# Kernel tuning notes

Hardware: AMD Instinct MI355X
Metric: run time of the kernel (lower is better)

Reference implementation:

```python
import jax, jax.numpy as jnp
import numpy as np

N_QUBITS = 10
DIM = 2 ** N_QUBITS
N_TOKENS = 32
LAYERS = 2
DEGREE = 3
VOCAB = 32000
EMB = 512
N_PARAMS = 4 * N_QUBITS * LAYERS      # angles per token circuit
N_PARAMS_FF = 4 * N_QUBITS            # quantum feedforward (1 layer)
BATCH = 32


def _ry(state, wire, theta, n):
    # state: [B, 2**n] complex64; theta: [B] float32. RY = [[c,-s],[s,c]], c=cos(th/2)
    st = state.reshape(-1, 2 ** wire, 2, 2 ** (n - wire - 1))
    c = jnp.cos(theta / 2)[:, None, None]
    s = jnp.sin(theta / 2)[:, None, None]
    a, b = st[:, :, 0, :], st[:, :, 1, :]
    st = jnp.stack([c * a - s * b, s * a + c * b], axis=2)
    return st.reshape(-1, 2 ** n)


def _crx(state, ctrl, tgt, theta, n):
    # controlled-RX: apply RX=[[c,-i s],[-i s,c]] on tgt where ctrl bit == 1
    lo, hi = (ctrl, tgt) if ctrl < tgt else (tgt, ctrl)
    st = state.reshape(-1, 2 ** lo, 2, 2 ** (hi - lo - 1), 2, 2 ** (n - hi - 1))
    caxis = 2 if ctrl < tgt else 4
    taxis = 4 if ctrl < tgt else 2
    c = jnp.cos(theta / 2).reshape(-1, 1, 1, 1, 1, 1)
    s = jnp.sin(theta / 2).reshape(-1, 1, 1, 1, 1, 1)
    c0 = jax.lax.index_in_dim(st, 0, caxis, keepdims=True)
    c1 = jax.lax.index_in_dim(st, 1, caxis, keepdims=True)
    a = jax.lax.index_in_dim(c1, 0, taxis, keepdims=True)
    b = jax.lax.index_in_dim(c1, 1, taxis, keepdims=True)
    na = c * a - 1j * s * b
    nb = -1j * s * a + c * b
    c1 = jnp.concatenate([na, nb], axis=taxis)
    st = jnp.concatenate([c0, c1], axis=caxis)
    return st.reshape(-1, 2 ** n)


def _ansatz14(state, params, n, layers):
    # gate order of ansatz 14 (arXiv:1905.10876); params: [B, 4*n*layers]
    idx = 0
    for _ in range(layers):
        for i in range(n):
            state = _ry(state, i, params[:, idx], n); idx += 1
        for i in range(n - 1, -1, -1):
            state = _crx(state, i, (i + 1) % n, params[:, idx], n); idx += 1
        for i in range(n):
            state = _ry(state, i, params[:, idx], n); idx += 1
        for i in [n - 1] + list(range(n - 1)):
            state = _crx(state, i, (i - 1) % n, params[:, idx], n); idx += 1
    return state


def _measure_xyz(state, n):
    # expectation of X,Y,Z on every wire; output [B, 3*n] ordered [x..., y..., z...]
    B = state.shape[0]
    xs, ys, zs = [], [], []
    for w in range(n):
        st = state.reshape(B, 2 ** w, 2, 2 ** (n - w - 1))
        a, b = st[:, :, 0, :], st[:, :, 1, :]
        z = jnp.sum(jnp.conj(a) * b, axis=(1, 2))
        xs.append(2.0 * jnp.real(z))
        ys.append(2.0 * jnp.imag(z))
        zs.append(jnp.sum(jnp.real(a * jnp.conj(a)) - jnp.real(b * jnp.conj(b)), axis=(1, 2)))
    return jnp.stack(xs + ys + zs, axis=1)


def _forward(x, emb, w_ang, b_ang, qsvt_coeffs, lcu_re, lcu_im, qff_params, w1, b1, w2, b2):
    B, T = x.shape
    lcu = (lcu_re + 1j * lcu_im).astype(jnp.complex64)
    lcu = lcu / jnp.maximum(jnp.sum(jnp.abs(lcu)), 1e-12)          # p=1 normalize
    angles = (emb[x] @ w_ang.T + b_ang).reshape(B * T, N_PARAMS)   # [B*T, P]
    init = jnp.zeros((B, DIM), jnp.complex64).at[:, 0].set(1.0)
    acc = qsvt_coeffs[0] * init
    mono = init
    for k in range(1, DEGREE + 1):
        rep = jnp.repeat(mono, T, axis=0)                          # [B*T, D]
        st = _ansatz14(rep, angles, N_QUBITS, LAYERS).reshape(B, T, DIM)
        mono = jnp.einsum('bwi,w->bi', st, lcu)                    # LCU combine
        acc = acc + qsvt_coeffs[k] * mono
    qsvt_state = acc / jnp.sum(jnp.abs(qsvt_coeffs))
    norm = jnp.linalg.norm(qsvt_state, axis=-1, keepdims=True)
    normed = qsvt_state / jnp.maximum(norm, 1e-12)
    qff = jnp.broadcast_to(qff_params[None, :], (B, N_PARAMS_FF))
    st2 = _ansatz14(normed, qff, N_QUBITS, 1)
    ev = _measure_xyz(st2, N_QUBITS)                               # [B, 3*nq]
    h = jax.nn.relu(ev @ w1.T + b1)
    logits = h @ w2.T + b2
    return logits, jnp.mean(norm[:, 0])


def setup_inputs() -> dict:
    key = jax.random.key(0)
    ks = jax.random.split(key, 9)
    return {
        'x': jax.random.randint(ks[0], (BATCH, N_TOKENS), 0, VOCAB, dtype=jnp.int32),
        'emb': jax.random.normal(ks[1], (VOCAB, EMB), jnp.float32) * 0.02,
        'w_ang': jax.random.normal(ks[2], (N_PARAMS, EMB), jnp.float32) * (1.0 / np.sqrt(EMB)),
        'b_ang': jnp.zeros((N_PARAMS,), jnp.float32),
        'qsvt_coeffs': jax.random.uniform(ks[3], (DEGREE + 1,), jnp.float32),
        'lcu_re': jax.random.uniform(ks[4], (N_TOKENS,), jnp.float32),
        'lcu_im': jax.random.uniform(ks[5], (N_TOKENS,), jnp.float32),
        'qff_params': jax.random.uniform(ks[6], (N_PARAMS_FF,), jnp.float32),
        'w1': jax.random.normal(ks[7], (EMB, 3 * N_QUBITS), jnp.float32) * (1.0 / np.sqrt(3 * N_QUBITS)),
        'b1': jnp.zeros((EMB,), jnp.float32),
        'w2': jax.random.normal(ks[8], (VOCAB, EMB), jnp.float32) * (1.0 / np.sqrt(EMB)),
        'b2': jnp.zeros((VOCAB,), jnp.float32),
    }


def reference(x, emb, w_ang, b_ang, qsvt_coeffs, lcu_re, lcu_im, qff_params, w1, b1, w2, b2):
    return _forward(x, emb, w_ang, b_ang, qsvt_coeffs, lcu_re, lcu_im, qff_params, w1, b1, w2, b2)
```

## Files before the change

### kernel.cpp

```cpp
#include <hip/hip_runtime.h>
#include <math.h>

#define DEV __device__ __forceinline__

namespace {

struct C2 { float x, y; };

constexpr size_t OFF_CS   = 0;
constexpr size_t OFF_NRM  = 163988;
constexpr size_t OFF_MONO = 164096;
constexpr size_t OFF_ACC  = 229632;
constexpr size_t OFF_ST   = 295168;
constexpr size_t OFF_H    = 2393280;


template<int P>
DEV void ry_gate(C2 v[16], int lane, float c, float s) {
  if constexpr (P >= 6) {
    constexpr int rm = 1 << (P - 6);
#pragma unroll
    for (int r = 0; r < 16; ++r) {
      if ((r & rm) == 0) {
        C2 a = v[r], b = v[r | rm];
        v[r].x      = fmaf(c, a.x, -s * b.x);
        v[r].y      = fmaf(c, a.y, -s * b.y);
        v[r | rm].x = fmaf(s, a.x,  c * b.x);
        v[r | rm].y = fmaf(s, a.y,  c * b.y);
      }
    }
  } else {
    constexpr int lm = 1 << P;
    float sg = (lane & lm) ? s : -s;
#pragma unroll
    for (int r = 0; r < 16; ++r) {
      float px = __shfl_xor(v[r].x, lm, 64);
      float py = __shfl_xor(v[r].y, lm, 64);
      v[r].x = fmaf(c, v[r].x, sg * px);
      v[r].y = fmaf(c, v[r].y, sg * py);
    }
  }
}

template<int PC, int PT>
DEV void crx_gate(C2 v[16], int lane, float c, float s) {
  if constexpr (PT >= 6) {
    constexpr int tm = 1 << (PT - 6);
#pragma unroll
    for (int r = 0; r < 16; ++r) {
      if ((r & tm) == 0) {
        if constexpr (PC >= 6) {
          constexpr int cm = 1 << (PC - 6);
          if ((r & cm) != 0) {
            C2 a = v[r], b = v[r | tm];
            v[r].x      = fmaf(c, a.x,  s * b.y);
            v[r].y      = fmaf(c, a.y, -s * b.x);
            v[r | tm].x = fmaf(c, b.x,  s * a.y);
            v[r | tm].y = fmaf(c, b.y, -s * a.x);
          }
        } else {
          constexpr int cl = 1 << PC;
          bool ct = (lane & cl) != 0;
          C2 a = v[r], b = v[r | tm];
          float nax = fmaf(c, a.x,  s * b.y);
          float nay = fmaf(c, a.y, -s * b.x);
          float nbx = fmaf(c, b.x,  s * a.y);
          float nby = fmaf(c, b.y, -s * a.x);
          v[r].x      = ct ? nax : a.x;
          v[r].y      = ct ? nay : a.y;
          v[r | tm].x = ct ? nbx : b.x;
          v[r | tm].y = ct ? nby : b.y;
        }
      }
    }
  } else {
    constexpr int tm = 1 << PT;
#pragma unroll
    for (int r = 0; r < 16; ++r) {
      if constexpr (PC >= 6) {
        constexpr int cm = 1 << (PC - 6);
        if ((r & cm) == 0) continue;
      }
      float px = __shfl_xor(v[r].x, tm, 64);
      float py = __shfl_xor(v[r].y, tm, 64);
      float nx = fmaf(c, v[r].x,  s * py);
      float ny = fmaf(c, v[r].y, -s * px);
      if constexpr (PC >= 6) {
        v[r].x = nx; v[r].y = ny;
      } else {
        constexpr int cl = 1 << PC;
        bool ct = (lane & cl) != 0;
        v[r].x = ct ? nx : v[r].x;
        v[r].y = ct ? ny : v[r].y;
      }
    }
  }
}

#define RYG(w, g)       ry_gate<9-(w)>(v, lane, cs[2*(g)], cs[2*(g)+1])
#define CRXG(cw, tw, g) crx_gate<9-(cw), 9-(tw)>(v, lane, cs[2*(g)], cs[2*(g)+1])

DEV void apply_layer(C2 v[16], int lane, const float* __restrict__ cs) {
  RYG(0,0); RYG(1,1); RYG(2,2); RYG(3,3); RYG(4,4);
  RYG(5,5); RYG(6,6); RYG(7,7); RYG(8,8); RYG(9,9);
  CRXG(9,0,10); CRXG(8,9,11); CRXG(7,8,12); CRXG(6,7,13); CRXG(5,6,14);
  CRXG(4,5,15); CRXG(3,4,16); CRXG(2,3,17); CRXG(1,2,18); CRXG(0,1,19);
  RYG(0,20); RYG(1,21); RYG(2,22); RYG(3,23); RYG(4,24);
  RYG(5,25); RYG(6,26); RYG(7,27); RYG(8,28); RYG(9,29);
  CRXG(9,8,30); CRXG(0,9,31); CRXG(1,0,32); CRXG(2,1,33); CRXG(3,2,34);
  CRXG(4,3,35); CRXG(5,4,36); CRXG(6,5,37); CRXG(7,6,38); CRXG(8,7,39);
}

template<int P>
DEV void measure_wire(const C2 v[16], int lane, float* ev, int w) {
  float x = 0.f, y = 0.f, z = 0.f;
  if constexpr (P >= 6) {
    constexpr int rm = 1 << (P - 6);
#pragma unroll
    for (int r = 0; r < 16; ++r) {
      if ((r & rm) == 0) {
        C2 a = v[r], b = v[r | rm];
        x += a.x*b.x + a.y*b.y;
        y += a.x*b.y - a.y*b.x;
        z += (a.x*a.x + a.y*a.y) - (b.x*b.x + b.y*b.y);
      }
    }
  } else {
    constexpr int lm = 1 << P;
#pragma unroll
    for (int r = 0; r < 16; ++r) {
      float px = __shfl_xor(v[r].x, lm, 64);
      float py = __shfl_xor(v[r].y, lm, 64);
      if ((lane & lm) == 0) {
        C2 a = v[r];
        x += a.x*px + a.y*py;
        y += a.x*py - a.y*px;
        z += (a.x*a.x + a.y*a.y) - (px*px + py*py);
      }
    }
  }
  for (int s = 1; s < 64; s <<= 1) {
    x += __shfl_xor(x, s, 64);
    y += __shfl_xor(y, s, 64);
    z += __shfl_xor(z, s, 64);
  }
  if (lane == 0) {
    ev[w]      = 2.f * x;
    ev[10 + w] = 2.f * y;
    ev[20 + w] = z;
  }
}

DEV void measure_all(const C2 v[16], int lane, float* ev) {
  measure_wire<9>(v, lane, ev, 0);
  measure_wire<8>(v, lane, ev, 1);
  measure_wire<7>(v, lane, ev, 2);
  measure_wire<6>(v, lane, ev, 3);
  measure_wire<5>(v, lane, ev, 4);
  measure_wire<4>(v, lane, ev, 5);
  measure_wire<3>(v, lane, ev, 6);
  measure_wire<2>(v, lane, ev, 7);
  measure_wire<1>(v, lane, ev, 8);
  measure_wire<0>(v, lane, ev, 9);
}


__global__ __launch_bounds__(128) void k_angles(const int* __restrict__ x,
                                                const float* __restrict__ emb,
                                                const float* __restrict__ w_ang,
                                                const float* __restrict__ b_ang,
                                                float* __restrict__ ws) {
  __shared__ float4 e4[4][128];
  int g = blockIdx.x;
  int tid = threadIdx.x;
#pragma unroll
  for (int rr = 0; rr < 4; ++rr) {
    int row = x[4 * g + rr];
    e4[rr][tid] = ((const float4*)(emb + (size_t)row * 512))[tid];
  }
  __syncthreads();
  if (tid < 80) {
    const float4* wr = (const float4*)(w_ang + (size_t)tid * 512);
    float bv = b_ang[tid];
    float a0 = bv, a1 = bv, a2 = bv, a3 = bv;
#pragma unroll 4
    for (int j = 0; j < 128; ++j) {
      float4 w = wr[j];
      float4 e0 = e4[0][j], e1 = e4[1][j], e2 = e4[2][j], e3 = e4[3][j];
      a0 = fmaf(w.x, e0.x, a0); a0 = fmaf(w.y, e0.y, a0);
      a0 = fmaf(w.z, e0.z, a0); a0 = fmaf(w.w, e0.w, a0);
      a1 = fmaf(w.x, e1.x, a1); a1 = fmaf(w.y, e1.y, a1);
      a1 = fmaf(w.z, e1.z, a1); a1 = fmaf(w.w, e1.w, a1);
      a2 = fmaf(w.x, e2.x, a2); a2 = fmaf(w.y, e2.y, a2);
      a2 = fmaf(w.z, e2.z, a2); a2 = fmaf(w.w, e2.w, a2);
      a3 = fmaf(w.x, e3.x, a3); a3 = fmaf(w.y, e3.y, a3);
      a3 = fmaf(w.z, e3.z, a3); a3 = fmaf(w.w, e3.w, a3);
    }
    float t0 = 0.5f * a0, t1 = 0.5f * a1, t2 = 0.5f * a2, t3 = 0.5f * a3;
    size_t base = OFF_CS + (size_t)(4 * g) * 160 + 2 * tid;
    ws[base]           = cosf(t0); ws[base + 1]       = sinf(t0);
    ws[base + 160]     = cosf(t1); ws[base + 161]     = sinf(t1);
    ws[base + 320]     = cosf(t2); ws[base + 321]     = sinf(t2);
    ws[base + 480]     = cosf(t3); ws[base + 481]     = sinf(t3);
  }
}

__global__ __launch_bounds__(256) void k_evolve(float* __restrict__ ws,
                                                const float* __restrict__ lr,
                                                const float* __restrict__ li,
                                                int k) {
  __shared__ float cs_lds[640];
  int tid = threadIdx.x;
  const float* csg = ws + OFF_CS + (size_t)blockIdx.x * 640;
  for (int i = tid; i < 640; i += 256) cs_lds[i] = csg[i];
  __syncthreads();
  int wid = tid >> 6, lane = tid & 63;
  int state = blockIdx.x * 4 + wid;
  int b = state >> 5, t = state & 31;

  float lre_v = 0.f, lim_v = 0.f;
  if (lane < 32) { lre_v = lr[lane]; lim_v = li[lane]; }
  float ab = sqrtf(lre_v * lre_v + lim_v * lim_v);
  for (int s = 1; s < 64; s <<= 1) ab += __shfl_xor(ab, s, 64);
  float invL = 1.f / fmaxf(ab, 1e-12f);
  float wre = __shfl(lre_v, t, 64) * invL;
  float wim = __shfl(lim_v, t, 64) * invL;

  C2 v[16];
  if (k == 1) {
#pragma unroll
    for (int r = 0; r < 16; ++r) {
      v[r].x = (r == 0 && lane == 0) ? 1.f : 0.f;
      v[r].y = 0.f;
    }
  } else {
    const float2* mono = (const float2*)(ws + OFF_MONO) + (size_t)b * 1024;
#pragma unroll
    for (int r = 0; r < 16; ++r) {
      float2 m = mono[(r << 6) | lane];
      v[r].x = m.x; v[r].y = m.y;
    }
  }
  const float* csw = &cs_lds[wid * 160];
  apply_layer(v, lane, csw);
  apply_layer(v, lane, csw + 80);
  float2* st = (float2*)(ws + OFF_ST) + (size_t)state * 1024;
#pragma unroll
  for (int r = 0; r < 16; ++r) {
    st[(r << 6) | lane] = make_float2(wre * v[r].x - wim * v[r].y,
                                      wre * v[r].y + wim * v[r].x);
  }
}

__global__ void k_reduce(float* __restrict__ ws, const float* __restrict__ coef, int k) {
  int idx = blockIdx.x * 256 + threadIdx.x;
  int b = idx >> 10, i = idx & 1023;
  const float2* st = (const float2*)(ws + OFF_ST) + (size_t)b * 32768 + i;
  float sx = 0.f, sy = 0.f;
#pragma unroll
  for (int t = 0; t < 32; ++t) {
    float2 vv = st[t * 1024];
    sx += vv.x; sy += vv.y;
  }
  float2* mono = (float2*)(ws + OFF_MONO);
  float2* acc  = (float2*)(ws + OFF_ACC);
  float ck = coef[k];
  if (k == 1) {
    float e0 = (i == 0) ? coef[0] : 0.f;
    acc[idx] = make_float2(fmaf(ck, sx, e0), ck * sy);
    mono[idx] = make_float2(sx, sy);
  } else {
    float2 a = acc[idx];
    a.x = fmaf(ck, sx, a.x);
    a.y = fmaf(ck, sy, a.y);
    acc[idx] = a;
    mono[idx] = make_float2(sx, sy);
  }
}

__global__ __launch_bounds__(256) void k_final(float* __restrict__ ws,
                                               const float* __restrict__ coef,
                                               const float* __restrict__ qff,
                                               const float* __restrict__ w1,
                                               const float* __restrict__ b1) {
  __shared__ float qff_lds[80];
  __shared__ float2 sv[1024];
  __shared__ float ev_lds[30];
  int tid = threadIdx.x;
  int b = blockIdx.x;
  if (tid < 40) {
    float th = 0.5f * qff[tid];
    qff_lds[2 * tid]     = cosf(th);
    qff_lds[2 * tid + 1] = sinf(th);
  }
  float den = fabsf(coef[0]) + fabsf(coef[1]) + fabsf(coef[2]) + fabsf(coef[3]);
  float invd = 1.f / den;
  float c3 = coef[3];
  const float2* stb  = (const float2*)(ws + OFF_ST) + (size_t)b * 32768;
  const float2* accb = (const float2*)(ws + OFF_ACC) + (size_t)b * 1024;
#pragma unroll
  for (int q = 0; q < 4; ++q) {
    int i = tid + q * 256;
    float sx = 0.f, sy = 0.f;
#pragma unroll
    for (int t = 0; t < 32; ++t) {
      float2 vv = stb[t * 1024 + i];
      sx += vv.x; sy += vv.y;
    }
    float2 a = accb[i];
    sv[i] = make_float2(fmaf(c3, sx, a.x) * invd, fmaf(c3, sy, a.y) * invd);
  }
  __syncthreads();
  if (tid < 64) {
    int lane = tid;
    C2 v[16];
    float ssum = 0.f;
#pragma unroll
    for (int r = 0; r < 16; ++r) {
      float2 m = sv[(r << 6) | lane];
      v[r].x = m.x; v[r].y = m.y;
      ssum += v[r].x * v[r].x + v[r].y * v[r].y;
    }
    for (int s = 1; s < 64; s <<= 1) ssum += __shfl_xor(ssum, s, 64);
    float nrm = sqrtf(ssum);
    if (lane == 0) ws[OFF_NRM + b] = nrm;
    float sc = 1.f / fmaxf(nrm, 1e-12f);
#pragma unroll
    for (int r = 0; r < 16; ++r) { v[r].x *= sc; v[r].y *= sc; }
    apply_layer(v, lane, qff_lds);
    measure_all(v, lane, ev_lds);
  }
  __syncthreads();
#pragma unroll
  for (int jj = 0; jj < 2; ++jj) {
    int j = tid + jj * 256;
    const float* wr = w1 + (size_t)j * 30;
    float a = b1[j];
#pragma unroll
    for (int q = 0; q < 30; ++q) a = fmaf(ev_lds[q], wr[q], a);
    ws[OFF_H + b * 512 + j] = fmaxf(a, 0.f);
  }
}

__global__ __launch_bounds__(256) void k_logits(const float* __restrict__ ws,
                                                const float* __restrict__ w2,
                                                const float* __restrict__ b2,
                                                float* __restrict__ out) {
  __shared__ float4 hT[4096];
  int tid = threadIdx.x;
  if (blockIdx.x == 0 && tid == 0) {
    float s = 0.f;
    for (int i = 0; i < 32; ++i) s += ws[OFF_NRM + i];
    out[32000u * 32u] = s * (1.f / 32.f);
  }
  const float4* hg = (const float4*)(ws + OFF_H);
#pragma unroll
  for (int p = 0; p < 16; ++p) {
    int idx = tid + p * 256;
    int m = idx >> 7, kf4 = idx & 127;
    hT[m * 128 + (kf4 ^ (m >> 3))] = hg[idx];
  }
  __syncthreads();

  int wv = tid >> 6, lane = tid & 63;
  int mg = lane & 3, nl = lane >> 2;
  int nbase = blockIdx.x * 64;
  float acc[4][8];
#pragma unroll
  for (int j = 0; j < 4; ++j)
#pragma unroll
    for (int mi = 0; mi < 8; ++mi) acc[j][mi] = 0.f;

  const float* wbase = w2 + (size_t)(nbase + nl * 4) * 512 + wv * 128;
  int kqb = wv * 32;
#pragma unroll 2
  for (int kf4 = 0; kf4 < 32; ++kf4) {
    int kcol = kqb + kf4;
    float4 h4[8];
#pragma unroll
    for (int mi = 0; mi < 8; ++mi) {
      int m = mg * 8 + mi;
      h4[mi] = hT[m * 128 + (kcol ^ mg)];
    }
#pragma unroll
    for (int j = 0; j < 4; ++j) {
      float4 w4 = *(const float4*)(wbase + (size_t)j * 512 + kf4 * 4);
#pragma unroll
      for (int mi = 0; mi < 8; ++mi) {
        acc[j][mi] = fmaf(w4.x, h4[mi].x, acc[j][mi]);
        acc[j][mi] = fmaf(w4.y, h4[mi].y, acc[j][mi]);
        acc[j][mi] = fmaf(w4.z, h4[mi].z, acc[j][mi]);
        acc[j][mi] = fmaf(w4.w, h4[mi].w, acc[j][mi]);
      }
    }
  }

  __syncthreads();
#pragma unroll
  for (int mi = 0; mi < 8; ++mi) {
    hT[wv * 512 + lane * 8 + (mi ^ (lane & 7))] =
        make_float4(acc[0][mi], acc[1][mi], acc[2][mi], acc[3][mi]);
  }
  __syncthreads();
  {
    int lane2 = tid & 63, grp = tid >> 6;
    int mg2 = lane2 & 3, nl2 = lane2 >> 2;
#pragma unroll
    for (int jj = 0; jj < 2; ++jj) {
      int mi2 = grp * 2 + jj;
      float4 s0 = hT[0 * 512 + lane2 * 8 + (mi2 ^ (lane2 & 7))];
      float4 s1 = hT[1 * 512 + lane2 * 8 + (mi2 ^ (lane2 & 7))];
      float4 s2 = hT[2 * 512 + lane2 * 8 + (mi2 ^ (lane2 & 7))];
      float4 s3 = hT[3 * 512 + lane2 * 8 + (mi2 ^ (lane2 & 7))];
      float sx = s0.x + s1.x + s2.x + s3.x;
      float sy = s0.y + s1.y + s2.y + s3.y;
      float sz = s0.z + s1.z + s2.z + s3.z;
      float sw = s0.w + s1.w + s2.w + s3.w;
      int m = mg2 * 8 + mi2;
      int col = nbase + nl2 * 4;
      float4 b2v = *(const float4*)(b2 + col);
      float4 res = make_float4(sx + b2v.x, sy + b2v.y, sz + b2v.z, sw + b2v.w);
      *(float4*)(out + (size_t)m * 32000 + col) = res;
    }
  }
}

}

extern "C" void kernel_launch(void* const* d_in, const int* in_sizes, int n_in,
                              void* d_out, int out_size, void* d_ws, size_t ws_size,
                              hipStream_t stream) {
  (void)in_sizes; (void)n_in; (void)out_size; (void)ws_size;
  const int*   x    = (const int*)d_in[0];
  const float* emb  = (const float*)d_in[1];
  const float* wang = (const float*)d_in[2];
  const float* bang = (const float*)d_in[3];
  const float* coef = (const float*)d_in[4];
  const float* lre  = (const float*)d_in[5];
  const float* lim  = (const float*)d_in[6];
  const float* qff  = (const float*)d_in[7];
  const float* w1   = (const float*)d_in[8];
  const float* b1   = (const float*)d_in[9];
  const float* w2   = (const float*)d_in[10];
  const float* b2   = (const float*)d_in[11];
  float* out = (float*)d_out;
  float* ws  = (float*)d_ws;

  hipLaunchKernelGGL(k_angles, dim3(256), dim3(128), 0, stream, x, emb, wang, bang, ws);
  hipLaunchKernelGGL(k_evolve, dim3(256), dim3(256), 0, stream, ws, lre, lim, 1);
  hipLaunchKernelGGL(k_reduce, dim3(128), dim3(256), 0, stream, ws, coef, 1);
  hipLaunchKernelGGL(k_evolve, dim3(256), dim3(256), 0, stream, ws, lre, lim, 2);
  hipLaunchKernelGGL(k_reduce, dim3(128), dim3(256), 0, stream, ws, coef, 2);
  hipLaunchKernelGGL(k_evolve, dim3(256), dim3(256), 0, stream, ws, lre, lim, 3);
  hipLaunchKernelGGL(k_final,  dim3(32),  dim3(256), 0, stream, ws, coef, qff, w1, b1);
  hipLaunchKernelGGL(k_logits, dim3(500), dim3(256), 0, stream, ws, w2, b2, out);
}
```

Before: 165.4 us.

## Split each state across two wavefronts and fuse angle computation into first evolve

Each 1024-amplitude state now spans two wavefronts (8 registers per lane instead of 16), with top-wire gates handled by exchanging halves through shared memory behind block barriers. The angle projection kernel is folded into the first evolve launch, which computes cos/sin into LDS and also writes them to the workspace for later passes. This doubles the thread count per state and cuts register pressure, trading that for extra LDS traffic and __syncthreads per layer, and it removes one launch.

```diff
diff --git a/kernel.cpp b/kernel.cpp
--- a/kernel.cpp
+++ b/kernel.cpp
@@ -13,7 +13,6 @@
 constexpr size_t OFF_ACC  = 229632;
 constexpr size_t OFF_ST   = 295168;
 constexpr size_t OFF_H    = 2393280;
-
 
 template<int P>
 DEV void ry_gate(C2 v[16], int lane, float c, float s) {
@@ -165,58 +164,253 @@
 }
 
 
-__global__ __launch_bounds__(128) void k_angles(const int* __restrict__ x,
-                                                const float* __restrict__ emb,
-                                                const float* __restrict__ w_ang,
-                                                const float* __restrict__ b_ang,
-                                                float* __restrict__ ws) {
-  __shared__ float4 e4[4][128];
-  int g = blockIdx.x;
-  int tid = threadIdx.x;
-#pragma unroll
-  for (int rr = 0; rr < 4; ++rr) {
-    int row = x[4 * g + rr];
-    e4[rr][tid] = ((const float4*)(emb + (size_t)row * 512))[tid];
-  }
+template<int P>
+DEV void ry8(C2 v[8], int lane, float c, float s) {
+  if constexpr (P >= 6) {
+    constexpr int rm = 1 << (P - 6);
+#pragma unroll
+    for (int r = 0; r < 8; ++r) {
+      if ((r & rm) == 0) {
+        C2 a = v[r], b = v[r | rm];
+        v[r].x      = fmaf(c, a.x, -s * b.x);
+        v[r].y      = fmaf(c, a.y, -s * b.y);
+        v[r | rm].x = fmaf(s, a.x,  c * b.x);
+        v[r | rm].y = fmaf(s, a.y,  c * b.y);
+      }
+    }
+  } else {
+    constexpr int lm = 1 << P;
+    float sg = (lane & lm) ? s : -s;
+#pragma unroll
+    for (int r = 0; r < 8; ++r) {
+      float px = __shfl_xor(v[r].x, lm, 64);
+      float py = __shfl_xor(v[r].y, lm, 64);
+      v[r].x = fmaf(c, v[r].x, sg * px);
+      v[r].y = fmaf(c, v[r].y, sg * py);
+    }
+  }
+}
+
+template<int PT>
+DEV void rx_all8(C2 v[8], int lane, float c, float s) {
+  if constexpr (PT >= 6) {
+    constexpr int tm = 1 << (PT - 6);
+#pragma unroll
+    for (int r = 0; r < 8; ++r) {
+      if ((r & tm) == 0) {
+        C2 a = v[r], bb = v[r | tm];
+        v[r].x      = fmaf(c, a.x,  s * bb.y);
+        v[r].y      = fmaf(c, a.y, -s * bb.x);
+        v[r | tm].x = fmaf(c, bb.x,  s * a.y);
+        v[r | tm].y = fmaf(c, bb.y, -s * a.x);
+      }
+    }
+  } else {
+    constexpr int tm = 1 << PT;
+#pragma unroll
+    for (int r = 0; r < 8; ++r) {
+      float px = __shfl_xor(v[r].x, tm, 64);
+      float py = __shfl_xor(v[r].y, tm, 64);
+      v[r].x = fmaf(c, v[r].x,  s * py);
+      v[r].y = fmaf(c, v[r].y, -s * px);
+    }
+  }
+}
+
+template<int PC, int PT>
+DEV void crx8(C2 v[8], int lane, int half, float c, float s) {
+  if constexpr (PC == 9) {
+    if (half) rx_all8<PT>(v, lane, c, s);
+  } else if constexpr (PT >= 6) {
+    constexpr int tm = 1 << (PT - 6);
+#pragma unroll
+    for (int r = 0; r < 8; ++r) {
+      if ((r & tm) == 0) {
+        if constexpr (PC >= 6) {
+          constexpr int cm = 1 << (PC - 6);
+          if ((r & cm) != 0) {
+            C2 a = v[r], bb = v[r | tm];
+            v[r].x      = fmaf(c, a.x,  s * bb.y);
+            v[r].y      = fmaf(c, a.y, -s * bb.x);
+            v[r | tm].x = fmaf(c, bb.x,  s * a.y);
+            v[r | tm].y = fmaf(c, bb.y, -s * a.x);
+          }
+        } else {
+          constexpr int cl = 1 << PC;
+          bool ct = (lane & cl) != 0;
+          C2 a = v[r], bb = v[r | tm];
+          float nax = fmaf(c, a.x,  s * bb.y);
+          float nay = fmaf(c, a.y, -s * bb.x);
+          float nbx = fmaf(c, bb.x,  s * a.y);
+          float nby = fmaf(c, bb.y, -s * a.x);
+          v[r].x      = ct ? nax : a.x;
+          v[r].y      = ct ? nay : a.y;
+          v[r | tm].x = ct ? nbx : bb.x;
+          v[r | tm].y = ct ? nby : bb.y;
+        }
+      }
+    }
+  } else {
+    constexpr int tm = 1 << PT;
+#pragma unroll
+    for (int r = 0; r < 8; ++r) {
+      if constexpr (PC >= 6) {
+        constexpr int cm = 1 << (PC - 6);
+        if ((r & cm) == 0) continue;
+      }
+      float px = __shfl_xor(v[r].x, tm, 64);
+      float py = __shfl_xor(v[r].y, tm, 64);
+      float nx = fmaf(c, v[r].x,  s * py);
+      float ny = fmaf(c, v[r].y, -s * px);
+      if constexpr (PC >= 6) {
+        v[r].x = nx; v[r].y = ny;
+      } else {
+        constexpr int cl = 1 << PC;
+        bool ct = (lane & cl) != 0;
+        v[r].x = ct ? nx : v[r].x;
+        v[r].y = ct ? ny : v[r].y;
+      }
+    }
+  }
+}
+
+DEV void xchg(float2 (*xb)[8][64], int wid, int lane, const C2 v[8], C2 p[8]) {
   __syncthreads();
-  if (tid < 80) {
-    const float4* wr = (const float4*)(w_ang + (size_t)tid * 512);
-    float bv = b_ang[tid];
-    float a0 = bv, a1 = bv, a2 = bv, a3 = bv;
+#pragma unroll
+  for (int r = 0; r < 8; ++r)
+    xb[wid][r][lane] = make_float2(v[r].x, v[r].y);
+  __syncthreads();
+#pragma unroll
+  for (int r = 0; r < 8; ++r) {
+    float2 q = xb[wid ^ 1][r][lane];
+    p[r].x = q.x; p[r].y = q.y;
+  }
+}
+
+DEV void ry_cross(C2 v[8], const C2 p[8], int half, float c, float s) {
+  float sg = half ? s : -s;
+#pragma unroll
+  for (int r = 0; r < 8; ++r) {
+    v[r].x = fmaf(c, v[r].x, sg * p[r].x);
+    v[r].y = fmaf(c, v[r].y, sg * p[r].y);
+  }
+}
+
+template<int CL>
+DEV void crx_cross_lane(C2 v[8], const C2 p[8], int lane, float c, float s) {
+#pragma unroll
+  for (int r = 0; r < 8; ++r) {
+    float nx = fmaf(c, v[r].x,  s * p[r].y);
+    float ny = fmaf(c, v[r].y, -s * p[r].x);
+    bool ct = (lane & CL) != 0;
+    v[r].x = ct ? nx : v[r].x;
+    v[r].y = ct ? ny : v[r].y;
+  }
+}
+
+DEV void crx_cross_reg(C2 v[8], const C2 p[8], float c, float s) {
+#pragma unroll
+  for (int r = 4; r < 8; ++r) {
+    v[r].x = fmaf(c, v[r].x,  s * p[r].y);
+    v[r].y = fmaf(c, v[r].y, -s * p[r].x);
+  }
+}
+
+DEV void apply_layer_split(C2 v[8], int lane, int half, int wid,
+                           const float* __restrict__ cs,
+                           float2 (*xb)[8][64]) {
+  C2 p[8];
+  xchg(xb, wid, lane, v, p);
+  ry_cross(v, p, half, cs[0], cs[1]);
+  ry8<8>(v, lane, cs[2],  cs[3]);
+  ry8<7>(v, lane, cs[4],  cs[5]);
+  ry8<6>(v, lane, cs[6],  cs[7]);
+  ry8<5>(v, lane, cs[8],  cs[9]);
+  ry8<4>(v, lane, cs[10], cs[11]);
+  ry8<3>(v, lane, cs[12], cs[13]);
+  ry8<2>(v, lane, cs[14], cs[15]);
+  ry8<1>(v, lane, cs[16], cs[17]);
+  ry8<0>(v, lane, cs[18], cs[19]);
+  xchg(xb, wid, lane, v, p);
+  crx_cross_lane<1>(v, p, lane, cs[20], cs[21]);
+  crx8<1,0>(v, lane, half, cs[22], cs[23]);
+  crx8<2,1>(v, lane, half, cs[24], cs[25]);
+  crx8<3,2>(v, lane, half, cs[26], cs[27]);
+  crx8<4,3>(v, lane, half, cs[28], cs[29]);
+  crx8<5,4>(v, lane, half, cs[30], cs[31]);
+  crx8<6,5>(v, lane, half, cs[32], cs[33]);
+  crx8<7,6>(v, lane, half, cs[34], cs[35]);
+  crx8<8,7>(v, lane, half, cs[36], cs[37]);
+  crx8<9,8>(v, lane, half, cs[38], cs[39]);
+  xchg(xb, wid, lane, v, p);
+  ry_cross(v, p, half, cs[40], cs[41]);
+  ry8<8>(v, lane, cs[42], cs[43]);
+  ry8<7>(v, lane, cs[44], cs[45]);
+  ry8<6>(v, lane, cs[46], cs[47]);
+  ry8<5>(v, lane, cs[48], cs[49]);
+  ry8<4>(v, lane, cs[50], cs[51]);
+  ry8<3>(v, lane, cs[52], cs[53]);
+  ry8<2>(v, lane, cs[54], cs[55]);
+  ry8<1>(v, lane, cs[56], cs[57]);
+  ry8<0>(v, lane, cs[58], cs[59]);
+  crx8<0,1>(v, lane, half, cs[60], cs[61]);
+  crx8<9,0>(v, lane, half, cs[62], cs[63]);
+  xchg(xb, wid, lane, v, p);
+  crx_cross_reg(v, p, cs[64], cs[65]);
+  crx8<7,8>(v, lane, half, cs[66], cs[67]);
+  crx8<6,7>(v, lane, half, cs[68], cs[69]);
+  crx8<5,6>(v, lane, half, cs[70], cs[71]);
+  crx8<4,5>(v, lane, half, cs[72], cs[73]);
+  crx8<3,4>(v, lane, half, cs[74], cs[75]);
+  crx8<2,3>(v, lane, half, cs[76], cs[77]);
+  crx8<1,2>(v, lane, half, cs[78], cs[79]);
+}
+
+
+template<int K>
+__global__ __launch_bounds__(512) void k_evolve(float* __restrict__ ws,
+    const float* __restrict__ lr, const float* __restrict__ li,
+    const int* __restrict__ x, const float* __restrict__ emb,
+    const float* __restrict__ w_ang, const float* __restrict__ b_ang) {
+  __shared__ float2 xbuf[8][8][64];
+  __shared__ float cs_lds[4][160];
+  const int tid = threadIdx.x, g = blockIdx.x;
+  const int wid = tid >> 6, lane = tid & 63;
+  const int sl = wid >> 1, half = wid & 1;
+  const int state = g * 4 + sl, b = state >> 5, t = state & 31;
+
+  if constexpr (K == 1) {
+    float* e4 = (float*)xbuf;
+    {
+      int rowi = tid >> 7, col = tid & 127;
+      int row = x[g * 4 + rowi];
+      ((float4*)e4)[rowi * 128 + col] =
+          ((const float4*)(emb + (size_t)row * 512))[col];
+    }
+    __syncthreads();
+    if (tid < 320) {
+      int tl = tid / 80, gate = tid - tl * 80;
+      const float4* wr = (const float4*)(w_ang + (size_t)gate * 512);
+      const float4* ep = (const float4*)e4 + (size_t)tl * 128;
+      float a = b_ang[gate];
 #pragma unroll 4
-    for (int j = 0; j < 128; ++j) {
-      float4 w = wr[j];
-      float4 e0 = e4[0][j], e1 = e4[1][j], e2 = e4[2][j], e3 = e4[3][j];
-      a0 = fmaf(w.x, e0.x, a0); a0 = fmaf(w.y, e0.y, a0);
-      a0 = fmaf(w.z, e0.z, a0); a0 = fmaf(w.w, e0.w, a0);
-      a1 = fmaf(w.x, e1.x, a1); a1 = fmaf(w.y, e1.y, a1);
-      a1 = fmaf(w.z, e1.z, a1); a1 = fmaf(w.w, e1.w, a1);
-      a2 = fmaf(w.x, e2.x, a2); a2 = fmaf(w.y, e2.y, a2);
-      a2 = fmaf(w.z, e2.z, a2); a2 = fmaf(w.w, e2.w, a2);
-      a3 = fmaf(w.x, e3.x, a3); a3 = fmaf(w.y, e3.y, a3);
-      a3 = fmaf(w.z, e3.z, a3); a3 = fmaf(w.w, e3.w, a3);
-    }
-    float t0 = 0.5f * a0, t1 = 0.5f * a1, t2 = 0.5f * a2, t3 = 0.5f * a3;
-    size_t base = OFF_CS + (size_t)(4 * g) * 160 + 2 * tid;
-    ws[base]           = cosf(t0); ws[base + 1]       = sinf(t0);
-    ws[base + 160]     = cosf(t1); ws[base + 161]     = sinf(t1);
-    ws[base + 320]     = cosf(t2); ws[base + 321]     = sinf(t2);
-    ws[base + 480]     = cosf(t3); ws[base + 481]     = sinf(t3);
-  }
-}
-
-__global__ __launch_bounds__(256) void k_evolve(float* __restrict__ ws,
-                                                const float* __restrict__ lr,
-                                                const float* __restrict__ li,
-                                                int k) {
-  __shared__ float cs_lds[640];
-  int tid = threadIdx.x;
-  const float* csg = ws + OFF_CS + (size_t)blockIdx.x * 640;
-  for (int i = tid; i < 640; i += 256) cs_lds[i] = csg[i];
-  __syncthreads();
-  int wid = tid >> 6, lane = tid & 63;
-  int state = blockIdx.x * 4 + wid;
-  int b = state >> 5, t = state & 31;
+      for (int j = 0; j < 128; ++j) {
+        float4 w4 = wr[j], e = ep[j];
+        a = fmaf(w4.x, e.x, a); a = fmaf(w4.y, e.y, a);
+        a = fmaf(w4.z, e.z, a); a = fmaf(w4.w, e.w, a);
+      }
+      float th = 0.5f * a, cv = cosf(th), sv = sinf(th);
+      cs_lds[tl][2 * gate]     = cv;
+      cs_lds[tl][2 * gate + 1] = sv;
+      size_t go = OFF_CS + (size_t)(g * 4 + tl) * 160 + 2 * gate;
+      ws[go] = cv; ws[go + 1] = sv;
+    }
+    __syncthreads();
+  } else {
+    const float* csg = ws + OFF_CS + (size_t)g * 640;
+    for (int i = tid; i < 640; i += 512) ((float*)cs_lds)[i] = csg[i];
+    __syncthreads();
+  }
 
   float lre_v = 0.f, lim_v = 0.f;
   if (lane < 32) { lre_v = lr[lane]; lim_v = li[lane]; }
@@ -226,27 +420,29 @@
   float wre = __shfl(lre_v, t, 64) * invL;
   float wim = __shfl(lim_v, t, 64) * invL;
 
-  C2 v[16];
-  if (k == 1) {
-#pragma unroll
-    for (int r = 0; r < 16; ++r) {
-      v[r].x = (r == 0 && lane == 0) ? 1.f : 0.f;
-      v[r].y = 0.f;
-    }
-  } else {
-    const float2* mono = (const float2*)(ws + OFF_MONO) + (size_t)b * 1024;
-#pragma unroll
-    for (int r = 0; r < 16; ++r) {
+  C2 v[8];
+  if constexpr (K == 1) {
+#pragma unroll
+    for (int r = 0; r < 8; ++r) { v[r].x = 0.f; v[r].y = 0.f; }
+    if (half == 0 && lane == 0) v[0].x = 1.f;
+  } else {
+    const float2* mono = (const float2*)(ws + OFF_MONO)
+                       + (size_t)b * 1024 + (half << 9);
+#pragma unroll
+    for (int r = 0; r < 8; ++r) {
       float2 m = mono[(r << 6) | lane];
       v[r].x = m.x; v[r].y = m.y;
     }
   }
-  const float* csw = &cs_lds[wid * 160];
-  apply_layer(v, lane, csw);
-  apply_layer(v, lane, csw + 80);
-  float2* st = (float2*)(ws + OFF_ST) + (size_t)state * 1024;
-#pragma unroll
-  for (int r = 0; r < 16; ++r) {
+
+  const float* cs0 = cs_lds[sl];
+  apply_layer_split(v, lane, half, wid, cs0, xbuf);
+  apply_layer_split(v, lane, half, wid, cs0 + 80, xbuf);
+
+  float2* st = (float2*)(ws + OFF_ST)
+             + (size_t)state * 1024 + (half << 9);
+#pragma unroll
+  for (int r = 0; r < 8; ++r) {
     st[(r << 6) | lane] = make_float2(wre * v[r].x - wim * v[r].y,
                                       wre * v[r].y + wim * v[r].x);
   }
@@ -446,12 +642,14 @@
   float* out = (float*)d_out;
   float* ws  = (float*)d_ws;
 
-  hipLaunchKernelGGL(k_angles, dim3(256), dim3(128), 0, stream, x, emb, wang, bang, ws);
-  hipLaunchKernelGGL(k_evolve, dim3(256), dim3(256), 0, stream, ws, lre, lim, 1);
+  hipLaunchKernelGGL(k_evolve<1>, dim3(256), dim3(512), 0, stream,
+                     ws, lre, lim, x, emb, wang, bang);
   hipLaunchKernelGGL(k_reduce, dim3(128), dim3(256), 0, stream, ws, coef, 1);
-  hipLaunchKernelGGL(k_evolve, dim3(256), dim3(256), 0, stream, ws, lre, lim, 2);
+  hipLaunchKernelGGL(k_evolve<2>, dim3(256), dim3(512), 0, stream,
+                     ws, lre, lim, x, emb, wang, bang);
   hipLaunchKernelGGL(k_reduce, dim3(128), dim3(256), 0, stream, ws, coef, 2);
-  hipLaunchKernelGGL(k_evolve, dim3(256), dim3(256), 0, stream, ws, lre, lim, 3);
+  hipLaunchKernelGGL(k_evolve<3>, dim3(256), dim3(512), 0, stream,
+                     ws, lre, lim, x, emb, wang, bang);
   hipLaunchKernelGGL(k_final,  dim3(32),  dim3(256), 0, stream, ws, coef, qff, w1, b1);
   hipLaunchKernelGGL(k_logits, dim3(500), dim3(256), 0, stream, ws, w2, b2, out);
 }
```

Measured after the change: 153.8 us. -7.1%, faster.

## Fuse angle projection into first evolve kernel and use DPP/swizzle lane exchanges

Applied to the files above, without the earlier changes.

The separate k_angles kernel is folded into a templated k_evolve<1>. It gathers embeddings, computes the cos/sin gate angles into LDS, and also writes them to the workspace for later passes, which removes one launch and the global round trip before the first evolve. The cross-lane butterfly exchanges for small lane masks now use DPP quad permutes and ds_swizzle instead of generic __shfl_xor, aiming for cheaper data movement in the gate and measurement loops. The fused kernel makes every thread do a 512-long dot product before evolving, which lengthens the first kernel.

```diff
diff --git a/kernel.cpp b/kernel.cpp
--- a/kernel.cpp
+++ b/kernel.cpp
@@ -14,6 +14,22 @@
 constexpr size_t OFF_ST   = 295168;
 constexpr size_t OFF_H    = 2393280;
 
+template<int LM>
+DEV float lxor(float x) {
+  if constexpr (LM == 1) {
+    return __int_as_float(__builtin_amdgcn_update_dpp(
+        __float_as_int(x), __float_as_int(x), 0xB1, 0xF, 0xF, false));
+  } else if constexpr (LM == 2) {
+    return __int_as_float(__builtin_amdgcn_update_dpp(
+        __float_as_int(x), __float_as_int(x), 0x4E, 0xF, 0xF, false));
+  } else if constexpr (LM == 4 || LM == 8 || LM == 16) {
+    return __int_as_float(__builtin_amdgcn_ds_swizzle(
+        __float_as_int(x), (LM << 10) | 0x1F));
+  } else {
+    return __shfl_xor(x, LM, 64);
+  }
+}
+
 
 template<int P>
 DEV void ry_gate(C2 v[16], int lane, float c, float s) {
@@ -34,8 +50,8 @@
     float sg = (lane & lm) ? s : -s;
 #pragma unroll
     for (int r = 0; r < 16; ++r) {
-      float px = __shfl_xor(v[r].x, lm, 64);
-      float py = __shfl_xor(v[r].y, lm, 64);
+      float px = lxor<lm>(v[r].x);
+      float py = lxor<lm>(v[r].y);
       v[r].x = fmaf(c, v[r].x, sg * px);
       v[r].y = fmaf(c, v[r].y, sg * py);
     }
@@ -81,8 +97,8 @@
         constexpr int cm = 1 << (PC - 6);
         if ((r & cm) == 0) continue;
       }
-      float px = __shfl_xor(v[r].x, tm, 64);
-      float py = __shfl_xor(v[r].y, tm, 64);
+      float px = lxor<tm>(v[r].x);
+      float py = lxor<tm>(v[r].y);
       float nx = fmaf(c, v[r].x,  s * py);
       float ny = fmaf(c, v[r].y, -s * px);
       if constexpr (PC >= 6) {
@@ -129,8 +145,8 @@
     constexpr int lm = 1 << P;
 #pragma unroll
     for (int r = 0; r < 16; ++r) {
-      float px = __shfl_xor(v[r].x, lm, 64);
-      float py = __shfl_xor(v[r].y, lm, 64);
+      float px = lxor<lm>(v[r].x);
+      float py = lxor<lm>(v[r].y);
       if ((lane & lm) == 0) {
         C2 a = v[r];
         x += a.x*px + a.y*py;
@@ -165,58 +181,53 @@
 }
 
 
-__global__ __launch_bounds__(128) void k_angles(const int* __restrict__ x,
-                                                const float* __restrict__ emb,
-                                                const float* __restrict__ w_ang,
-                                                const float* __restrict__ b_ang,
-                                                float* __restrict__ ws) {
-  __shared__ float4 e4[4][128];
-  int g = blockIdx.x;
-  int tid = threadIdx.x;
-#pragma unroll
-  for (int rr = 0; rr < 4; ++rr) {
-    int row = x[4 * g + rr];
-    e4[rr][tid] = ((const float4*)(emb + (size_t)row * 512))[tid];
-  }
-  __syncthreads();
-  if (tid < 80) {
-    const float4* wr = (const float4*)(w_ang + (size_t)tid * 512);
-    float bv = b_ang[tid];
-    float a0 = bv, a1 = bv, a2 = bv, a3 = bv;
+template<int K>
+__global__ __launch_bounds__(256) void k_evolve(float* __restrict__ ws,
+    const float* __restrict__ lr, const float* __restrict__ li,
+    const int* __restrict__ x, const float* __restrict__ emb,
+    const float* __restrict__ w_ang, const float* __restrict__ b_ang) {
+  __shared__ float cs_lds[4][160];
+  const int tid = threadIdx.x, g = blockIdx.x;
+  const int wid = tid >> 6, lane = tid & 63;
+  const int state = g * 4 + wid, b = state >> 5, t = state & 31;
+
+  if constexpr (K == 1) {
+    __shared__ float e4[4][512];
+#pragma unroll
+    for (int p = 0; p < 2; ++p) {
+      int idx = tid + p * 256;
+      int rr = idx >> 7, col = idx & 127;
+      int row = x[g * 4 + rr];
+      ((float4*)e4[rr])[col] = ((const float4*)(emb + (size_t)row * 512))[col];
+    }
+    __syncthreads();
+#pragma unroll
+    for (int p = 0; p < 2; ++p) {
+      int d = tid + p * 256;
+      if (d < 320) {
+        int tl = d / 80, gate = d - tl * 80;
+        const float4* wr = (const float4*)(w_ang + (size_t)gate * 512);
+        const float4* ep = (const float4*)e4[tl];
+        float a = b_ang[gate];
 #pragma unroll 4
-    for (int j = 0; j < 128; ++j) {
-      float4 w = wr[j];
-      float4 e0 = e4[0][j], e1 = e4[1][j], e2 = e4[2][j], e3 = e4[3][j];
-      a0 = fmaf(w.x, e0.x, a0); a0 = fmaf(w.y, e0.y, a0);
-      a0 = fmaf(w.z, e0.z, a0); a0 = fmaf(w.w, e0.w, a0);
-      a1 = fmaf(w.x, e1.x, a1); a1 = fmaf(w.y, e1.y, a1);
-      a1 = fmaf(w.z, e1.z, a1); a1 = fmaf(w.w, e1.w, a1);
-      a2 = fmaf(w.x, e2.x, a2); a2 = fmaf(w.y, e2.y, a2);
-      a2 = fmaf(w.z, e2.z, a2); a2 = fmaf(w.w, e2.w, a2);
-      a3 = fmaf(w.x, e3.x, a3); a3 = fmaf(w.y, e3.y, a3);
-      a3 = fmaf(w.z, e3.z, a3); a3 = fmaf(w.w, e3.w, a3);
-    }
-    float t0 = 0.5f * a0, t1 = 0.5f * a1, t2 = 0.5f * a2, t3 = 0.5f * a3;
-    size_t base = OFF_CS + (size_t)(4 * g) * 160 + 2 * tid;
-    ws[base]           = cosf(t0); ws[base + 1]       = sinf(t0);
-    ws[base + 160]     = cosf(t1); ws[base + 161]     = sinf(t1);
-    ws[base + 320]     = cosf(t2); ws[base + 321]     = sinf(t2);
-    ws[base + 480]     = cosf(t3); ws[base + 481]     = sinf(t3);
-  }
-}
-
-__global__ __launch_bounds__(256) void k_evolve(float* __restrict__ ws,
-                                                const float* __restrict__ lr,
-                                                const float* __restrict__ li,
-                                                int k) {
-  __shared__ float cs_lds[640];
-  int tid = threadIdx.x;
-  const float* csg = ws + OFF_CS + (size_t)blockIdx.x * 640;
-  for (int i = tid; i < 640; i += 256) cs_lds[i] = csg[i];
-  __syncthreads();
-  int wid = tid >> 6, lane = tid & 63;
-  int state = blockIdx.x * 4 + wid;
-  int b = state >> 5, t = state & 31;
+        for (int j = 0; j < 128; ++j) {
+          float4 w4 = wr[j], e = ep[j];
+          a = fmaf(w4.x, e.x, a); a = fmaf(w4.y, e.y, a);
+          a = fmaf(w4.z, e.z, a); a = fmaf(w4.w, e.w, a);
+        }
+        float th = 0.5f * a, cv = cosf(th), sv = sinf(th);
+        cs_lds[tl][2 * gate]     = cv;
+        cs_lds[tl][2 * gate + 1] = sv;
+        size_t go = OFF_CS + (size_t)(g * 4 + tl) * 160 + 2 * gate;
+        ws[go] = cv; ws[go + 1] = sv;
+      }
+    }
+    __syncthreads();
+  } else {
+    const float* csg = ws + OFF_CS + (size_t)g * 640;
+    for (int i = tid; i < 640; i += 256) ((float*)cs_lds)[i] = csg[i];
+    __syncthreads();
+  }
 
   float lre_v = 0.f, lim_v = 0.f;
   if (lane < 32) { lre_v = lr[lane]; lim_v = li[lane]; }
@@ -227,7 +238,7 @@
   float wim = __shfl(lim_v, t, 64) * invL;
 
   C2 v[16];
-  if (k == 1) {
+  if constexpr (K == 1) {
 #pragma unroll
     for (int r = 0; r < 16; ++r) {
       v[r].x = (r == 0 && lane == 0) ? 1.f : 0.f;
@@ -241,9 +252,11 @@
       v[r].x = m.x; v[r].y = m.y;
     }
   }
-  const float* csw = &cs_lds[wid * 160];
+
+  const float* csw = cs_lds[wid];
   apply_layer(v, lane, csw);
   apply_layer(v, lane, csw + 80);
+
   float2* st = (float2*)(ws + OFF_ST) + (size_t)state * 1024;
 #pragma unroll
   for (int r = 0; r < 16; ++r) {
@@ -446,12 +459,14 @@
   float* out = (float*)d_out;
   float* ws  = (float*)d_ws;
 
-  hipLaunchKernelGGL(k_angles, dim3(256), dim3(128), 0, stream, x, emb, wang, bang, ws);
-  hipLaunchKernelGGL(k_evolve, dim3(256), dim3(256), 0, stream, ws, lre, lim, 1);
+  hipLaunchKernelGGL(k_evolve<1>, dim3(256), dim3(256), 0, stream,
+                     ws, lre, lim, x, emb, wang, bang);
   hipLaunchKernelGGL(k_reduce, dim3(128), dim3(256), 0, stream, ws, coef, 1);
-  hipLaunchKernelGGL(k_evolve, dim3(256), dim3(256), 0, stream, ws, lre, lim, 2);
+  hipLaunchKernelGGL(k_evolve<2>, dim3(256), dim3(256), 0, stream,
+                     ws, lre, lim, x, emb, wang, bang);
   hipLaunchKernelGGL(k_reduce, dim3(128), dim3(256), 0, stream, ws, coef, 2);
-  hipLaunchKernelGGL(k_evolve, dim3(256), dim3(256), 0, stream, ws, lre, lim, 3);
+  hipLaunchKernelGGL(k_evolve<3>, dim3(256), dim3(256), 0, stream,
+                     ws, lre, lim, x, emb, wang, bang);
   hipLaunchKernelGGL(k_final,  dim3(32),  dim3(256), 0, stream, ws, coef, qff, w1, b1);
   hipLaunchKernelGGL(k_logits, dim3(500), dim3(256), 0, stream, ws, w2, b2, out);
 }
```

Measured after the change: 149.0 us. 1.11x faster.
